# Performance work log

Hardware: AMD Instinct MI355X
Metric: run time of the kernel (lower is better)

## Reference

```python
import jax, jax.numpy as jnp
import numpy as np

N = 200000          # nodes
G = 8192            # graphs (data.num_graphs)
NUM_RADIAL = 32
M_OUT = 85          # embedding_depth // 3 -> 85x1o


def setup_inputs() -> dict:
    key = jax.random.key(0)
    ks = jax.random.split(key, 24)
    f32 = jnp.float32
    def rn(k, shape, scale=1.0):
        return jax.random.normal(k, shape, dtype=f32) * scale
    inp = {}
    inp['pos'] = rn(ks[0], (N, 3))
    inp['z'] = jax.random.randint(ks[1], (N,), 0, 100)
    inp['batch'] = jnp.sort(jax.random.randint(ks[2], (N,), 0, G))
    inp['node_table'] = rn(ks[3], (100, 32))
    # MLP weights (fan-in scaled), biases zero
    inp['W_rbf0'] = rn(ks[4], (32, 64), 32 ** -0.5)
    inp['b_rbf0'] = jnp.zeros((64,), f32)
    inp['W_rbf1'] = rn(ks[5], (64, 64), 64 ** -0.5)
    inp['b_rbf1'] = jnp.zeros((64,), f32)
    inp['W_m0'] = rn(ks[6], (96, 64), 96 ** -0.5)
    inp['b_m0'] = jnp.zeros((64,), f32)
    inp['W_m1'] = rn(ks[7], (64, 64), 64 ** -0.5)
    inp['b_m1'] = jnp.zeros((64,), f32)
    inp['W_m2'] = rn(ks[8], (64, 64), 64 ** -0.5)
    inp['b_m2'] = jnp.zeros((64,), f32)
    # e3nn-style weights: N(0,1), path normalization applied in the math
    inp['w_tp0'] = rn(ks[9], (64, 64))   # 0e x 0e -> 0e
    inp['w_tp1'] = rn(ks[10], (64, 64))  # 0e x 1o -> 1o
    inp['w_tp2'] = rn(ks[11], (64, 32))  # 0e x 2e -> 2e
    inp['L0'] = rn(ks[12], (64, 64))     # o3.Linear 0e block
    inp['L1o'] = rn(ks[13], (64, 64))    # o3.Linear 1o block
    inp['L2e'] = rn(ks[14], (32, 32))    # o3.Linear 2e block
    inp['L_out'] = rn(ks[15], (64, 85))  # tl2: 64x1o -> 85x1o
    return inp


def _sph_harm(pos):
    # e3nn real spherical harmonics, normalize=False, normalization='component'
    x, y, z = pos[:, 0], pos[:, 1], pos[:, 2]
    sh0 = jnp.ones_like(x)                              # [N]     l=0
    sh1 = jnp.sqrt(3.0) * pos                           # [N,3]   l=1
    s15 = jnp.sqrt(15.0)
    s5 = jnp.sqrt(5.0)
    sh2 = jnp.stack([
        s15 * x * z,
        s15 * x * y,
        s5 * (y * y - 0.5 * (x * x + z * z)),
        s15 * y * z,
        0.5 * s15 * (z * z - x * x),
    ], axis=-1)                                          # [N,5]   l=2
    return sh0, sh1, sh2


def _forward(pos, z, batch, node_table, W_rbf0, b_rbf0, W_rbf1, b_rbf1,
             W_m0, b_m0, W_m1, b_m1, W_m2, b_m2,
             w_tp0, w_tp1, w_tp2, L0, L1o, L2e, L_out):
    sh0, sh1, sh2 = _sph_harm(pos)  # centroid is zeros

    # Gaussian RBF on |pos|, start=0 stop=1
    dist = jnp.linalg.norm(pos, axis=1)                  # [N]
    offsets = jnp.linspace(0.0, 1.0, NUM_RADIAL)
    coeff = -0.5 / (offsets[1] - offsets[0]) ** 2
    rbf = jnp.exp(coeff * (dist[:, None] - offsets) ** 2)  # [N,32]

    # rbf_emb MLP (1 hidden layer)
    r = jax.nn.gelu(rbf @ W_rbf0 + b_rbf0)
    r = r @ W_rbf1 + b_rbf1                               # [N,64]

    # radial_message MLP (2 hidden layers) on [r_emb, node_emb]
    h = jnp.concatenate([r, node_table[z]], axis=-1)      # [N,96]
    h = jax.nn.gelu(h @ W_m0 + b_m0)
    h = jax.nn.gelu(h @ W_m1 + b_m1)
    msg = h @ W_m2 + b_m2                                 # [N,64]  64x0e

    # FullyConnectedTensorProduct(64x0e, 1x0e+1x1o+1x2e -> irreps_mid)
    # scalar (x) l  -> l ; path norm 1/sqrt(fan_in), fan_in = 64*1
    inv = 1.0 / jnp.sqrt(64.0)
    c0 = (msg @ w_tp0) * sh0[:, None] * inv               # [N,64]    0e
    c1 = (msg @ w_tp1)[:, :, None] * sh1[:, None, :] * inv  # [N,64,3] 1o
    c2 = (msg @ w_tp2)[:, :, None] * sh2[:, None, :] * inv  # [N,32,5] 2e
    # 64x1e and 32x2o output blocks have no allowed paths -> identically zero

    # act1: gelu on scalar (0e) irreps only
    c0 = jax.nn.gelu(c0)

    # scatter mean + scatter sum over graphs
    cnt = jnp.maximum(jax.ops.segment_sum(jnp.ones_like(dist), batch, num_segments=G), 1.0)
    def agg(v, cshape):
        s = jax.ops.segment_sum(v, batch, num_segments=G)
        return s / cnt.reshape(cshape) + s
    g0 = agg(c0, (G, 1))        # [G,64]
    g1 = agg(c1, (G, 1, 1))     # [G,64,3]
    g2 = agg(c2, (G, 1, 1))     # [G,32,5]

    # tl1 (o3.Linear, per-irrep multiplicity mixing, 1/sqrt(mult_in) norm)
    g0 = g0 @ L0 * (64 ** -0.5)
    g1 = jnp.einsum('gum,uv->gvm', g1, L1o) * (64 ** -0.5)
    g2 = jnp.einsum('gum,uv->gvm', g2, L2e) * (32 ** -0.5)

    # act2: gelu on 0e only (g0 subsequently dropped by tl2's 1o-only output)
    g0 = jax.nn.gelu(g0)

    # tl2: irreps_mid -> 85x1o; only the 1o block contributes
    enc = jnp.einsum('gum,uv->gvm', g1, L_out) * (64 ** -0.5)  # [G,85,3]
    return enc.reshape(G, M_OUT * 3)


def reference(pos, z, batch, node_table, W_rbf0, b_rbf0, W_rbf1, b_rbf1,
              W_m0, b_m0, W_m1, b_m1, W_m2, b_m2,
              w_tp0, w_tp1, w_tp2, L0, L1o, L2e, L_out):
    return _forward(pos, z, batch, node_table, W_rbf0, b_rbf0, W_rbf1, b_rbf1,
                    W_m0, b_m0, W_m1, b_m1, W_m2, b_m2,
                    w_tp0, w_tp1, w_tp2, L0, L1o, L2e, L_out)
```

## Files before the change

kernel.cpp:

```cpp
#include <hip/hip_runtime.h>


typedef __attribute__((ext_vector_type(8))) short bf16x8;
typedef __attribute__((ext_vector_type(4))) float f32x4;
typedef unsigned short ushort_t;

#define SBW 72

__device__ __forceinline__ unsigned rnebits(float x) {
    unsigned u = __float_as_uint(x);
    return u + 0x7fffu + ((u >> 16) & 1u);
}
__device__ __forceinline__ ushort_t f2bf(float x) { return (ushort_t)(rnebits(x) >> 16); }
__device__ __forceinline__ float bf2f(ushort_t h) { return __uint_as_float(((unsigned)h) << 16); }
__device__ __forceinline__ unsigned pack2bf(float lo, float hi) {
    return (rnebits(hi) & 0xffff0000u) | (rnebits(lo) >> 16);
}
__device__ __forceinline__ void ds_order_fence() {
    __builtin_amdgcn_sched_barrier(0x7F);
}

__device__ __forceinline__ float gelu(float x) {
    float x2 = x * x;
    float y  = x * fmaf(0.10294324f, x2, 2.3022082f);
    float e  = __builtin_amdgcn_exp2f(y);
    float r  = __builtin_amdgcn_rcpf(e + 1.0f);
    return fmaf(-x, r, x);
}

__global__ __launch_bounds__(256)
void prep_kernel(const float* __restrict__ W_rbf0, const float* __restrict__ W_rbf1,
                 const float* __restrict__ W_m0, const float* __restrict__ W_m1,
                 const float* __restrict__ W_m2, const float* __restrict__ b_m0,
                 const float* __restrict__ b_m2, const float* __restrict__ w_tp1,
                 const float* __restrict__ L1o, const float* __restrict__ L_out,
                 const float* __restrict__ node_table, const int* __restrict__ batch,
                 ushort_t* __restrict__ wb, float* __restrict__ tblc,
                 float* __restrict__ bc, float* __restrict__ Lcomb,
                 int* __restrict__ seg, int N, int G)
{
    if (blockIdx.x >= 127) {
        int i = (blockIdx.x - 127) * 256 + threadIdx.x;
        if (i >= N) return;
        int bi = batch[i];
        int bprev = (i == 0) ? -1 : batch[i - 1];
        for (int g = bprev + 1; g <= bi; ++g) seg[g] = i;
        if (i == N - 1) for (int g = bi + 1; g <= G; ++g) seg[g] = N;
        return;
    }
    int idx = blockIdx.x * 256 + threadIdx.x;
    float w;
    ushort_t *dh, *dl;
    if (idx < 4096) {
        int f = idx >> 6, k = idx & 63;
        w = (k < 32) ? W_rbf0[k * 64 + f] : 0.0f;
        dh = wb + idx; dl = wb + 4096 + idx;
    } else if (idx < 8192) {
        int j = idx - 4096, f = j >> 6, k = j & 63;
        w = W_rbf1[k * 64 + f]; dh = wb + 8192 + j; dl = wb + 12288 + j;
    } else if (idx < 12288) {
        int j = idx - 8192, f = j >> 6, k = j & 63;
        w = W_m0[k * 64 + f]; dh = wb + 16384 + j; dl = wb + 20480 + j;
    } else if (idx < 16384) {
        int j = idx - 12288, f = j >> 6, k = j & 63;
        w = W_m1[k * 64 + f]; dh = wb + 24576 + j; dl = wb + 28672 + j;
    } else if (idx < 20480) {
        int j = idx - 16384, f = j >> 6, k = j & 63;
        float s = 0.f;
        for (int jj = 0; jj < 64; ++jj) s = fmaf(W_m2[k * 64 + jj], w_tp1[jj * 64 + f], s);
        w = s; dh = wb + 32768 + j; dl = wb + 36864 + j;
    } else if (idx < 26880) {
        int j = idx - 20480, zz = j >> 6, f = j & 63;
        float s = b_m0[f];
        for (int k = 0; k < 32; ++k) s = fmaf(node_table[zz * 32 + k], W_m0[(64 + k) * 64 + f], s);
        tblc[j] = s;
        return;
    } else if (idx < 26944) {
        int b = idx - 26880;
        float s = 0.f;
        for (int k = 0; k < 64; ++k) s = fmaf(b_m2[k], w_tp1[k * 64 + b], s);
        bc[b] = s;
        return;
    } else if (idx < 32384) {
        int j = idx - 26944, u = j / 85, v = j - 85 * u;
        float s = 0.f;
        for (int k = 0; k < 64; ++k) s = fmaf(L1o[u * 64 + k], L_out[k * 85 + v], s);
        Lcomb[j] = 0.015625f * s;
        return;
    } else return;
    ushort_t h = f2bf(w);
    *dh = h;
    *dl = f2bf(w - bf2f(h));
}

__global__ __launch_bounds__(256, 4)
void node_mfma_kernel(const float* __restrict__ pos, const int* __restrict__ z,
                      const ushort_t* __restrict__ wb,
                      const float* __restrict__ tblc,
                      const float* __restrict__ b_rbf0, const float* __restrict__ b_rbf1,
                      const float* __restrict__ b_m1, const float* __restrict__ bc,
                      ushort_t* __restrict__ Tout, int N, int ntiles)
{
    __shared__ ushort_t bufs[4 * 64 * SBW];
    const int wid = threadIdx.x >> 6;
    const int lane = threadIdx.x & 63;
    const int tile = blockIdx.x * 4 + wid;
    if (tile >= ntiles) return;
    ushort_t* buf = bufs + wid * (64 * SBW);

    const int lrow = lane >> 4, lcol = lane & 15;
    const int nodebase = tile * 64;
    int gn = nodebase + lane;
    if (gn > N - 1) gn = N - 1;

    {
        const float px = pos[3 * gn], py = pos[3 * gn + 1], pz = pos[3 * gn + 2];
        const float dist = sqrtf(px * px + py * py + pz * pz);
        unsigned rb[16];
        #pragma unroll
        for (int j = 0; j < 16; ++j) {
            float d0 = dist - (float)(2 * j)     * (1.0f / 31.0f);
            float d1 = dist - (float)(2 * j + 1) * (1.0f / 31.0f);
            rb[j] = pack2bf(__builtin_amdgcn_exp2f(-693.2149671554846f * d0 * d0),
                            __builtin_amdgcn_exp2f(-693.2149671554846f * d1 * d1));
        }
        uint4* dst = (uint4*)&buf[lane * SBW];
        dst[0] = make_uint4(rb[0], rb[1], rb[2], rb[3]);
        dst[1] = make_uint4(rb[4], rb[5], rb[6], rb[7]);
        dst[2] = make_uint4(rb[8], rb[9], rb[10], rb[11]);
        dst[3] = make_uint4(rb[12], rb[13], rb[14], rb[15]);
        uint4 zz = make_uint4(0, 0, 0, 0);
        dst[4] = zz; dst[5] = zz; dst[6] = zz; dst[7] = zz;
    }
    int zn0, zn1, zn2, zn3;
    {
        int n0 = nodebase + 0  + lcol; if (n0 > N - 1) n0 = N - 1;
        int n1 = nodebase + 16 + lcol; if (n1 > N - 1) n1 = N - 1;
        int n2 = nodebase + 32 + lcol; if (n2 > N - 1) n2 = N - 1;
        int n3 = nodebase + 48 + lcol; if (n3 > N - 1) n3 = N - 1;
        zn0 = z[n0]; zn1 = z[n1]; zn2 = z[n2]; zn3 = z[n3];
    }
    ds_order_fence();

    #pragma unroll 1
    for (int L = 0; L < 5; ++L) {
        const ushort_t* whb = wb + L * 8192;
        f32x4 acc[4][4];
        if (L == 2) {
            const int zn[4] = {zn0, zn1, zn2, zn3};
            #pragma unroll
            for (int n = 0; n < 4; ++n) {
                const float* tp = tblc + zn[n] * 64 + lrow * 4;
                #pragma unroll
                for (int m = 0; m < 4; ++m) {
                    float4 bv = *(const float4*)(tp + m * 16);
                    acc[m][n][0] = bv.x; acc[m][n][1] = bv.y;
                    acc[m][n][2] = bv.z; acc[m][n][3] = bv.w;
                }
            }
        } else {
            const float* bp = (L == 0) ? b_rbf0 : (L == 1) ? b_rbf1 : (L == 3) ? b_m1 : bc;
            #pragma unroll
            for (int m = 0; m < 4; ++m) {
                float4 bv = *(const float4*)(bp + m * 16 + lrow * 4);
                #pragma unroll
                for (int n = 0; n < 4; ++n) {
                    acc[m][n][0] = bv.x; acc[m][n][1] = bv.y;
                    acc[m][n][2] = bv.z; acc[m][n][3] = bv.w;
                }
            }
        }
        #pragma unroll
        for (int kt = 0; kt < 2; ++kt) {
            const int kof = kt * 32 + lrow * 8;
            bf16x8 bb[4], ah[4], al[4];
            #pragma unroll
            for (int n = 0; n < 4; ++n)
                bb[n] = *(const bf16x8*)&buf[(n * 16 + lcol) * SBW + kof];
            #pragma unroll
            for (int m = 0; m < 4; ++m) {
                ah[m] = *(const bf16x8*)(whb + (m * 16 + lcol) * 64 + kof);
                al[m] = *(const bf16x8*)(whb + 4096 + (m * 16 + lcol) * 64 + kof);
            }
            #pragma unroll
            for (int m = 0; m < 4; ++m)
                #pragma unroll
                for (int n = 0; n < 4; ++n)
                    acc[m][n] = __builtin_amdgcn_mfma_f32_16x16x32_bf16(ah[m], bb[n], acc[m][n], 0, 0, 0);
            #pragma unroll
            for (int m = 0; m < 4; ++m)
                #pragma unroll
                for (int n = 0; n < 4; ++n)
                    acc[m][n] = __builtin_amdgcn_mfma_f32_16x16x32_bf16(al[m], bb[n], acc[m][n], 0, 0, 0);
        }
        ds_order_fence();
        if ((L == 0) | (L == 2) | (L == 3)) {
            #pragma unroll
            for (int m = 0; m < 4; ++m) {
                const int f0 = m * 16 + lrow * 4;
                #pragma unroll
                for (int n = 0; n < 4; ++n) {
                    f32x4 v = acc[m][n];
                    uint2 pk;
                    pk.x = pack2bf(gelu(v[0]), gelu(v[1]));
                    pk.y = pack2bf(gelu(v[2]), gelu(v[3]));
                    *(uint2*)&buf[(n * 16 + lcol) * SBW + f0] = pk;
                }
            }
        } else {
            #pragma unroll
            for (int m = 0; m < 4; ++m) {
                const int f0 = m * 16 + lrow * 4;
                #pragma unroll
                for (int n = 0; n < 4; ++n) {
                    f32x4 v = acc[m][n];
                    uint2 pk;
                    pk.x = pack2bf(v[0], v[1]);
                    pk.y = pack2bf(v[2], v[3]);
                    *(uint2*)&buf[(n * 16 + lcol) * SBW + f0] = pk;
                }
            }
        }
        ds_order_fence();
    }

    {
        ushort_t* tb2 = Tout + (size_t)nodebase * 64;
        #pragma unroll
        for (int i = 0; i < 8; ++i) {
            const int r = i * 8 + (lane >> 3);
            bf16x8 v = *(const bf16x8*)&buf[r * SBW + (lane & 7) * 8];
            if (nodebase + r < N)
                *(bf16x8*)(tb2 + i * 512 + lane * 8) = v;
        }
    }
}

__global__ __launch_bounds__(256)
void graph_kernel(const ushort_t* __restrict__ Tin, const float* __restrict__ pos,
                  const int* __restrict__ seg, const float* __restrict__ Lcomb,
                  float* __restrict__ out, int G) {
    __shared__ float g1s[4][64][3];
    const int lane = threadIdx.x & 63;
    const int wid = threadIdx.x >> 6;
    const int g = blockIdx.x * 4 + wid;
    const bool active = g < G;

    if (active) {
        const int s = seg[g], e = seg[g + 1];
        float a0 = 0.f, a1 = 0.f, a2 = 0.f;
        for (int nn = s; nn < e; ++nn) {
            float t = bf2f(Tin[(size_t)nn * 64 + lane]);
            float qx = pos[3 * nn + 0], qy = pos[3 * nn + 1], qz = pos[3 * nn + 2];
            a0 = fmaf(t, qx, a0);
            a1 = fmaf(t, qy, a1);
            a2 = fmaf(t, qz, a2);
        }
        float cnt = (float)((e - s) > 0 ? (e - s) : 1);
        float sc = 1.7320508075688772f * 0.125f * (1.0f + 1.0f / cnt);
        g1s[wid][lane][0] = a0 * sc;
        g1s[wid][lane][1] = a1 * sc;
        g1s[wid][lane][2] = a2 * sc;
    }
    __syncthreads();
    if (!active) return;

    float o0 = 0.f, o1 = 0.f, o2 = 0.f, p0 = 0.f, p1 = 0.f, p2 = 0.f;
    const int v2 = 64 + lane;
    for (int u = 0; u < 64; ++u) {
        float b0 = g1s[wid][u][0], b1 = g1s[wid][u][1], b2 = g1s[wid][u][2];
        float l0 = Lcomb[u * 85 + lane];
        o0 = fmaf(b0, l0, o0); o1 = fmaf(b1, l0, o1); o2 = fmaf(b2, l0, o2);
        if (lane < 21) {
            float l1 = Lcomb[u * 85 + v2];
            p0 = fmaf(b0, l1, p0); p1 = fmaf(b1, l1, p1); p2 = fmaf(b2, l1, p2);
        }
    }
    float* og = out + (size_t)g * 255;
    og[3 * lane + 0] = o0; og[3 * lane + 1] = o1; og[3 * lane + 2] = o2;
    if (lane < 21) {
        og[3 * v2 + 0] = p0; og[3 * v2 + 1] = p1; og[3 * v2 + 2] = p2;
    }
}

extern "C" void kernel_launch(void* const* d_in, const int* in_sizes, int n_in,
                              void* d_out, int out_size, void* d_ws, size_t ws_size,
                              hipStream_t stream) {
    const float* pos        = (const float*)d_in[0];
    const int*   z          = (const int*)d_in[1];
    const int*   batch      = (const int*)d_in[2];
    const float* node_table = (const float*)d_in[3];
    const float* W_rbf0     = (const float*)d_in[4];
    const float* b_rbf0     = (const float*)d_in[5];
    const float* W_rbf1     = (const float*)d_in[6];
    const float* b_rbf1     = (const float*)d_in[7];
    const float* W_m0       = (const float*)d_in[8];
    const float* b_m0       = (const float*)d_in[9];
    const float* W_m1       = (const float*)d_in[10];
    const float* b_m1       = (const float*)d_in[11];
    const float* W_m2       = (const float*)d_in[12];
    const float* b_m2       = (const float*)d_in[13];
    const float* w_tp1      = (const float*)d_in[15];
    const float* L1o        = (const float*)d_in[18];
    const float* L_out      = (const float*)d_in[20];
    float* out = (float*)d_out;

    const int N = in_sizes[0] / 3;
    const int G = out_size / 255;
    const int ntiles = (N + 63) / 64;

    char* ws = (char*)d_ws;
    float*    bc    = (float*)(ws + 0);
    float*    Lcomb = (float*)(ws + 256);
    int*      seg   = (int*)(ws + 22528);
    ushort_t* wb    = (ushort_t*)(ws + 55552);
    float*    tblc  = (float*)(ws + 137472);
    ushort_t* T     = (ushort_t*)(ws + 163072);

    const int segBlocks = (N + 255) / 256;
    prep_kernel<<<127 + segBlocks, 256, 0, stream>>>(
        W_rbf0, W_rbf1, W_m0, W_m1, W_m2, b_m0, b_m2, w_tp1, L1o, L_out,
        node_table, batch, wb, tblc, bc, Lcomb, seg, N, G);

    node_mfma_kernel<<<(ntiles + 3) / 4, 256, 0, stream>>>(
        pos, z, wb, tblc, b_rbf0, b_rbf1, b_m1, bc, T, N, ntiles);

    graph_kernel<<<(G + 3) / 4, 256, 0, stream>>>(T, pos, seg, Lcomb, out, G);
}
```

Before: 95.43 us.

## Fuse per-graph pos-weighted segment reduction into node kernel via atomics

The node MLP kernel now reduces its output features times node position directly into a per-graph float accumulator with atomicAdd, instead of writing a bf16 [N,64] intermediate that a graph kernel re-reads. Tiles shrink from 64 to 32 nodes per wave so there are twice as many waves. GELU is computed in pairs sharing one reciprocal, and packing uses the HIP bf16x2 conversion. This removes the intermediate global write and read, at the cost of a memset, atomic traffic, and a non-deterministic summation order.

```diff
diff --git a/kernel.cpp b/kernel.cpp
--- a/kernel.cpp
+++ b/kernel.cpp
@@ -1,4 +1,5 @@
 #include <hip/hip_runtime.h>
+#include <hip/hip_bf16.h>
 
 
 typedef __attribute__((ext_vector_type(8))) short bf16x8;
@@ -13,19 +14,24 @@
 }
 __device__ __forceinline__ ushort_t f2bf(float x) { return (ushort_t)(rnebits(x) >> 16); }
 __device__ __forceinline__ float bf2f(ushort_t h) { return __uint_as_float(((unsigned)h) << 16); }
-__device__ __forceinline__ unsigned pack2bf(float lo, float hi) {
-    return (rnebits(hi) & 0xffff0000u) | (rnebits(lo) >> 16);
+__device__ __forceinline__ unsigned pk2(float lo, float hi) {
+    __hip_bfloat162 h2 = __float22bfloat162_rn(make_float2(lo, hi));
+    unsigned r;
+    __builtin_memcpy(&r, &h2, 4);
+    return r;
 }
 __device__ __forceinline__ void ds_order_fence() {
     __builtin_amdgcn_sched_barrier(0x7F);
 }
 
-__device__ __forceinline__ float gelu(float x) {
-    float x2 = x * x;
-    float y  = x * fmaf(0.10294324f, x2, 2.3022082f);
-    float e  = __builtin_amdgcn_exp2f(y);
-    float r  = __builtin_amdgcn_rcpf(e + 1.0f);
-    return fmaf(-x, r, x);
+__device__ __forceinline__ void gelu2(float& a, float& b) {
+    float ya = fminf(a * fmaf(0.10294324f, a * a, 2.3022082f), 60.0f);
+    float yb = fminf(b * fmaf(0.10294324f, b * b, 2.3022082f), 60.0f);
+    float sa = __builtin_amdgcn_exp2f(ya) + 1.0f;
+    float sb = __builtin_amdgcn_exp2f(yb) + 1.0f;
+    float R  = __builtin_amdgcn_rcpf(sa * sb);
+    a = fmaf(-a, R * sb, a);
+    b = fmaf(-b, R * sa, b);
 }
 
 __global__ __launch_bounds__(256)
@@ -95,61 +101,63 @@
 
 __global__ __launch_bounds__(256, 4)
 void node_mfma_kernel(const float* __restrict__ pos, const int* __restrict__ z,
-                      const ushort_t* __restrict__ wb,
-                      const float* __restrict__ tblc,
+                      const int* __restrict__ batch,
+                      const ushort_t* __restrict__ wb, const float* __restrict__ tblc,
                       const float* __restrict__ b_rbf0, const float* __restrict__ b_rbf1,
                       const float* __restrict__ b_m1, const float* __restrict__ bc,
-                      ushort_t* __restrict__ Tout, int N, int ntiles)
+                      float* __restrict__ g1, int N, int ntiles)
 {
-    __shared__ ushort_t bufs[4 * 64 * SBW];
+    __shared__ ushort_t bufs[4 * 32 * SBW];
     const int wid = threadIdx.x >> 6;
     const int lane = threadIdx.x & 63;
     const int tile = blockIdx.x * 4 + wid;
     if (tile >= ntiles) return;
-    ushort_t* buf = bufs + wid * (64 * SBW);
+    ushort_t* buf = bufs + wid * (32 * SBW);
 
     const int lrow = lane >> 4, lcol = lane & 15;
-    const int nodebase = tile * 64;
-    int gn = nodebase + lane;
-    if (gn > N - 1) gn = N - 1;
-
+    const int nodebase = tile * 32;
+    const int nend = (N - nodebase) < 32 ? (N - nodebase) : 32;
+
+    float mypx, mypy, mypz;
+    int myb;
     {
-        const float px = pos[3 * gn], py = pos[3 * gn + 1], pz = pos[3 * gn + 2];
-        const float dist = sqrtf(px * px + py * py + pz * pz);
-        unsigned rb[16];
+        const int nd = lane & 31, half = lane >> 5;
+        int gn = nodebase + nd;
+        if (gn > N - 1) gn = N - 1;
+        mypx = pos[3 * gn]; mypy = pos[3 * gn + 1]; mypz = pos[3 * gn + 2];
+        myb  = batch[gn];
+        const float dist = sqrtf(mypx * mypx + mypy * mypy + mypz * mypz);
+        unsigned rb[8];
         #pragma unroll
-        for (int j = 0; j < 16; ++j) {
-            float d0 = dist - (float)(2 * j)     * (1.0f / 31.0f);
-            float d1 = dist - (float)(2 * j + 1) * (1.0f / 31.0f);
-            rb[j] = pack2bf(__builtin_amdgcn_exp2f(-693.2149671554846f * d0 * d0),
-                            __builtin_amdgcn_exp2f(-693.2149671554846f * d1 * d1));
-        }
-        uint4* dst = (uint4*)&buf[lane * SBW];
+        for (int j = 0; j < 8; ++j) {
+            float d0 = dist - (float)(half * 16 + 2 * j)     * (1.0f / 31.0f);
+            float d1 = dist - (float)(half * 16 + 2 * j + 1) * (1.0f / 31.0f);
+            rb[j] = pk2(__builtin_amdgcn_exp2f(-693.2149671554846f * d0 * d0),
+                        __builtin_amdgcn_exp2f(-693.2149671554846f * d1 * d1));
+        }
+        uint4* dst = (uint4*)&buf[nd * SBW + half * 16];
         dst[0] = make_uint4(rb[0], rb[1], rb[2], rb[3]);
         dst[1] = make_uint4(rb[4], rb[5], rb[6], rb[7]);
-        dst[2] = make_uint4(rb[8], rb[9], rb[10], rb[11]);
-        dst[3] = make_uint4(rb[12], rb[13], rb[14], rb[15]);
-        uint4 zz = make_uint4(0, 0, 0, 0);
-        dst[4] = zz; dst[5] = zz; dst[6] = zz; dst[7] = zz;
-    }
-    int zn0, zn1, zn2, zn3;
+        uint4* dz = (uint4*)&buf[nd * SBW + 32 + half * 16];
+        dz[0] = make_uint4(0, 0, 0, 0);
+        dz[1] = make_uint4(0, 0, 0, 0);
+    }
+    int zn0, zn1;
     {
         int n0 = nodebase + 0  + lcol; if (n0 > N - 1) n0 = N - 1;
         int n1 = nodebase + 16 + lcol; if (n1 > N - 1) n1 = N - 1;
-        int n2 = nodebase + 32 + lcol; if (n2 > N - 1) n2 = N - 1;
-        int n3 = nodebase + 48 + lcol; if (n3 > N - 1) n3 = N - 1;
-        zn0 = z[n0]; zn1 = z[n1]; zn2 = z[n2]; zn3 = z[n3];
+        zn0 = z[n0]; zn1 = z[n1];
     }
     ds_order_fence();
 
     #pragma unroll 1
     for (int L = 0; L < 5; ++L) {
         const ushort_t* whb = wb + L * 8192;
-        f32x4 acc[4][4];
+        f32x4 acc[4][2];
         if (L == 2) {
-            const int zn[4] = {zn0, zn1, zn2, zn3};
-            #pragma unroll
-            for (int n = 0; n < 4; ++n) {
+            const int zn[2] = {zn0, zn1};
+            #pragma unroll
+            for (int n = 0; n < 2; ++n) {
                 const float* tp = tblc + zn[n] * 64 + lrow * 4;
                 #pragma unroll
                 for (int m = 0; m < 4; ++m) {
@@ -164,7 +172,7 @@
             for (int m = 0; m < 4; ++m) {
                 float4 bv = *(const float4*)(bp + m * 16 + lrow * 4);
                 #pragma unroll
-                for (int n = 0; n < 4; ++n) {
+                for (int n = 0; n < 2; ++n) {
                     acc[m][n][0] = bv.x; acc[m][n][1] = bv.y;
                     acc[m][n][2] = bv.z; acc[m][n][3] = bv.w;
                 }
@@ -173,9 +181,9 @@
         #pragma unroll
         for (int kt = 0; kt < 2; ++kt) {
             const int kof = kt * 32 + lrow * 8;
-            bf16x8 bb[4], ah[4], al[4];
-            #pragma unroll
-            for (int n = 0; n < 4; ++n)
+            bf16x8 bb[2], ah[4], al[4];
+            #pragma unroll
+            for (int n = 0; n < 2; ++n)
                 bb[n] = *(const bf16x8*)&buf[(n * 16 + lcol) * SBW + kof];
             #pragma unroll
             for (int m = 0; m < 4; ++m) {
@@ -185,61 +193,60 @@
             #pragma unroll
             for (int m = 0; m < 4; ++m)
                 #pragma unroll
-                for (int n = 0; n < 4; ++n)
+                for (int n = 0; n < 2; ++n)
                     acc[m][n] = __builtin_amdgcn_mfma_f32_16x16x32_bf16(ah[m], bb[n], acc[m][n], 0, 0, 0);
             #pragma unroll
             for (int m = 0; m < 4; ++m)
                 #pragma unroll
-                for (int n = 0; n < 4; ++n)
+                for (int n = 0; n < 2; ++n)
                     acc[m][n] = __builtin_amdgcn_mfma_f32_16x16x32_bf16(al[m], bb[n], acc[m][n], 0, 0, 0);
         }
         ds_order_fence();
-        if ((L == 0) | (L == 2) | (L == 3)) {
-            #pragma unroll
-            for (int m = 0; m < 4; ++m) {
-                const int f0 = m * 16 + lrow * 4;
-                #pragma unroll
-                for (int n = 0; n < 4; ++n) {
-                    f32x4 v = acc[m][n];
-                    uint2 pk;
-                    pk.x = pack2bf(gelu(v[0]), gelu(v[1]));
-                    pk.y = pack2bf(gelu(v[2]), gelu(v[3]));
-                    *(uint2*)&buf[(n * 16 + lcol) * SBW + f0] = pk;
-                }
-            }
-        } else {
-            #pragma unroll
-            for (int m = 0; m < 4; ++m) {
-                const int f0 = m * 16 + lrow * 4;
-                #pragma unroll
-                for (int n = 0; n < 4; ++n) {
-                    f32x4 v = acc[m][n];
-                    uint2 pk;
-                    pk.x = pack2bf(v[0], v[1]);
-                    pk.y = pack2bf(v[2], v[3]);
-                    *(uint2*)&buf[(n * 16 + lcol) * SBW + f0] = pk;
-                }
+        const bool act = (L == 0) | (L == 2) | (L == 3);
+        #pragma unroll
+        for (int m = 0; m < 4; ++m) {
+            const int f0 = m * 16 + lrow * 4;
+            #pragma unroll
+            for (int n = 0; n < 2; ++n) {
+                f32x4 v = acc[m][n];
+                float v0 = v[0], v1 = v[1], v2 = v[2], v3 = v[3];
+                if (act) { gelu2(v0, v1); gelu2(v2, v3); }
+                uint2 pk;
+                pk.x = pk2(v0, v1);
+                pk.y = pk2(v2, v3);
+                *(uint2*)&buf[(n * 16 + lcol) * SBW + f0] = pk;
             }
         }
         ds_order_fence();
     }
 
     {
-        ushort_t* tb2 = Tout + (size_t)nodebase * 64;
-        #pragma unroll
-        for (int i = 0; i < 8; ++i) {
-            const int r = i * 8 + (lane >> 3);
-            bf16x8 v = *(const bf16x8*)&buf[r * SBW + (lane & 7) * 8];
-            if (nodebase + r < N)
-                *(bf16x8*)(tb2 + i * 512 + lane * 8) = v;
-        }
+        float a0 = 0.f, a1 = 0.f, a2 = 0.f;
+        int curg = __shfl(myb, 0);
+        for (int nd = 0; nd < nend; ++nd) {
+            int bg = __shfl(myb, nd);
+            if (bg != curg) {
+                atomicAdd(&g1[curg * 192 + lane],       a0);
+                atomicAdd(&g1[curg * 192 + 64 + lane],  a1);
+                atomicAdd(&g1[curg * 192 + 128 + lane], a2);
+                a0 = a1 = a2 = 0.f;
+                curg = bg;
+            }
+            float t = bf2f(buf[nd * SBW + lane]);
+            float qx = __shfl(mypx, nd), qy = __shfl(mypy, nd), qz = __shfl(mypz, nd);
+            a0 = fmaf(t, qx, a0);
+            a1 = fmaf(t, qy, a1);
+            a2 = fmaf(t, qz, a2);
+        }
+        atomicAdd(&g1[curg * 192 + lane],       a0);
+        atomicAdd(&g1[curg * 192 + 64 + lane],  a1);
+        atomicAdd(&g1[curg * 192 + 128 + lane], a2);
     }
 }
 
 __global__ __launch_bounds__(256)
-void graph_kernel(const ushort_t* __restrict__ Tin, const float* __restrict__ pos,
-                  const int* __restrict__ seg, const float* __restrict__ Lcomb,
-                  float* __restrict__ out, int G) {
+void graph_final(const float* __restrict__ g1, const int* __restrict__ seg,
+                 const float* __restrict__ Lcomb, float* __restrict__ out, int G) {
     __shared__ float g1s[4][64][3];
     const int lane = threadIdx.x & 63;
     const int wid = threadIdx.x >> 6;
@@ -247,20 +254,12 @@
     const bool active = g < G;
 
     if (active) {
-        const int s = seg[g], e = seg[g + 1];
-        float a0 = 0.f, a1 = 0.f, a2 = 0.f;
-        for (int nn = s; nn < e; ++nn) {
-            float t = bf2f(Tin[(size_t)nn * 64 + lane]);
-            float qx = pos[3 * nn + 0], qy = pos[3 * nn + 1], qz = pos[3 * nn + 2];
-            a0 = fmaf(t, qx, a0);
-            a1 = fmaf(t, qy, a1);
-            a2 = fmaf(t, qz, a2);
-        }
-        float cnt = (float)((e - s) > 0 ? (e - s) : 1);
+        int c = seg[g + 1] - seg[g];
+        float cnt = (float)(c > 0 ? c : 1);
         float sc = 1.7320508075688772f * 0.125f * (1.0f + 1.0f / cnt);
-        g1s[wid][lane][0] = a0 * sc;
-        g1s[wid][lane][1] = a1 * sc;
-        g1s[wid][lane][2] = a2 * sc;
+        g1s[wid][lane][0] = g1[g * 192 + lane] * sc;
+        g1s[wid][lane][1] = g1[g * 192 + 64 + lane] * sc;
+        g1s[wid][lane][2] = g1[g * 192 + 128 + lane] * sc;
     }
     __syncthreads();
     if (!active) return;
@@ -307,7 +306,7 @@
 
     const int N = in_sizes[0] / 3;
     const int G = out_size / 255;
-    const int ntiles = (N + 63) / 64;
+    const int ntiles = (N + 31) / 32;
 
     char* ws = (char*)d_ws;
     float*    bc    = (float*)(ws + 0);
@@ -315,7 +314,9 @@
     int*      seg   = (int*)(ws + 22528);
     ushort_t* wb    = (ushort_t*)(ws + 55552);
     float*    tblc  = (float*)(ws + 137472);
-    ushort_t* T     = (ushort_t*)(ws + 163072);
+    float*    g1    = (float*)(ws + 163072);
+
+    (void)hipMemsetAsync(g1, 0, (size_t)G * 192 * sizeof(float), stream);
 
     const int segBlocks = (N + 255) / 256;
     prep_kernel<<<127 + segBlocks, 256, 0, stream>>>(
@@ -323,7 +324,7 @@
         node_table, batch, wb, tblc, bc, Lcomb, seg, N, G);
 
     node_mfma_kernel<<<(ntiles + 3) / 4, 256, 0, stream>>>(
-        pos, z, wb, tblc, b_rbf0, b_rbf1, b_m1, bc, T, N, ntiles);
-
-    graph_kernel<<<(G + 3) / 4, 256, 0, stream>>>(T, pos, seg, Lcomb, out, G);
-}
+        pos, z, batch, wb, tblc, b_rbf0, b_rbf1, b_m1, bc, g1, N, ntiles);
+
+    graph_final<<<(G + 3) / 4, 256, 0, stream>>>(g1, seg, Lcomb, out, G);
+}
```

After: 114.0 us. 19.5% more time.
